# Performance work log

Hardware: AMD Instinct MI355X
Metric: run time of the kernel (lower is better)

Reference implementation:

```python
import jax, jax.numpy as jnp
import numpy as np

B, T, C, HR = 8, 4096, 256, 4
N_LAYER, LAYER_ID = 12, 3
HID = HR * C


def _fancy_decay_first():
    # Faithful reproduction of VRWKV_SpatialMix._init_weights(init_mode='fancy')
    r01 = LAYER_ID / (N_LAYER - 1)
    h = np.arange(C, dtype=np.float32)
    decay = -5.0 + 8.0 * (h / (C - 1)) ** (0.7 + 1.3 * r01)
    zig = ((np.arange(1, C + 1) % 3) - 1).astype(np.float32) * 0.5
    first = np.float32(np.log(0.3)) + zig
    return jnp.asarray(decay, jnp.float32), jnp.asarray(first, jnp.float32)


def setup_inputs() -> dict:
    key = jax.random.key(0)
    ks = jax.random.split(key, 12)
    s = 0.02  # small weight scale keeps exp(k) well-conditioned
    decay, first = _fancy_decay_first()
    return {
        "x": jax.random.normal(ks[0], (B, T, C), jnp.float32),
        "Wk": jax.random.normal(ks[1], (C, C), jnp.float32) * s,
        "Wv": jax.random.normal(ks[2], (C, C), jnp.float32) * s,
        "Wr": jax.random.normal(ks[3], (C, C), jnp.float32) * s,
        "Wo": jax.random.normal(ks[4], (C, C), jnp.float32) * s,
        "Wk_ffn": jax.random.normal(ks[5], (C, HID), jnp.float32) * s,
        "Wv_ffn": jax.random.normal(ks[6], (HID, C), jnp.float32) * s,
        "Wr_ffn": jax.random.normal(ks[7], (C, C), jnp.float32) * s,
        "g1": 1.0 + 0.1 * jax.random.normal(ks[8], (C,), jnp.float32),
        "b1": 0.1 * jax.random.normal(ks[9], (C,), jnp.float32),
        "g2": 1.0 + 0.1 * jax.random.normal(ks[10], (C,), jnp.float32),
        "b2": 0.1 * jax.random.normal(ks[11], (C,), jnp.float32),
        "spatial_decay": decay,
        "spatial_first": first,
    }


def _ln(x, g, b):
    m = jnp.mean(x, axis=-1, keepdims=True)
    v = jnp.var(x, axis=-1, keepdims=True)
    return (x - m) * jax.lax.rsqrt(v + 1e-5) * g + b


def _wkv(w, u, k, v):
    # Numerically-stable log-space WKV recurrence (same math as wkv_cuda):
    # y_t = (sum_{i<t} e^{w*(t-1-i)+k_i} v_i + e^{u+k_t} v_t)
    #     / (sum_{i<t} e^{w*(t-1-i)+k_i}     + e^{u+k_t})
    # w,u: [C]; k,v: [B,T,C] -> y: [B,T,C]
    Bb, Tt, Cc = k.shape
    kT = jnp.swapaxes(k, 0, 1)  # [T,B,C]
    vT = jnp.swapaxes(v, 0, 1)

    def step(carry, kv):
        p, q, o = carry           # [B,C] num / den / running max exponent
        kt, vt = kv               # [B,C]
        no = jnp.maximum(o, u + kt)
        A = jnp.exp(o - no)
        E = jnp.exp(u + kt - no)
        y = (A * p + E * vt) / (A * q + E)
        no2 = jnp.maximum(w + o, kt)
        A2 = jnp.exp(w + o - no2)
        E2 = jnp.exp(kt - no2)
        return (A2 * p + E2 * vt, A2 * q + E2, no2), y

    init = (jnp.zeros((Bb, Cc), k.dtype),
            jnp.zeros((Bb, Cc), k.dtype),
            jnp.full((Bb, Cc), -1e38, k.dtype))
    _, yT = jax.lax.scan(step, init, (kT, vT))
    return jnp.swapaxes(yT, 0, 1)


def reference(x, Wk, Wv, Wr, Wo, Wk_ffn, Wv_ffn, Wr_ffn, g1, b1, g2, b2,
              spatial_decay, spatial_first):
    Tlen = x.shape[1]
    # --- SpatialMix (shift_pixel=0 -> xk=xv=xr=h, key_norm=False) ---
    h = _ln(x, g1, b1)
    k = h @ Wk
    v = h @ Wv
    sr = jax.nn.sigmoid(h @ Wr)
    y = _wkv(spatial_decay / Tlen, spatial_first / Tlen, k, v)
    x = x + (sr * y) @ Wo
    # --- ChannelMix (square-ReLU MLP, sigmoid receptance gate) ---
    h2 = _ln(x, g2, b2)
    kk = jnp.square(jax.nn.relu(h2 @ Wk_ffn))
    x = x + jax.nn.sigmoid(h2 @ Wr_ffn) * (kk @ Wv_ffn)
    return x
```

## Files before the change

kernel.cpp:

```cpp
#include <hip/hip_runtime.h>
#include <hip/hip_bf16.h>
#include <math.h>

#define TDIM 4096
#define CDIM 256
#define BDIM 8
#define NTOK (BDIM * TDIM)
#define HIDDIM 1024
#define NCHUNK 256
#define CHLEN 16

typedef float f32x4 __attribute__((ext_vector_type(4)));
typedef __bf16 bf16x8 __attribute__((ext_vector_type(8)));
typedef __bf16 bf16x4 __attribute__((ext_vector_type(4)));
typedef long long i64x2 __attribute__((ext_vector_type(2)));

#define GLDS16(gp, lp) __builtin_amdgcn_global_load_lds( \
    (const __attribute__((address_space(1))) void*)(gp), \
    (__attribute__((address_space(3))) void*)(lp), 16, 0, 0)

#define WAITCNT_VM8  0x0F78
#define WAITCNT_VM5  0x0F75
#define WAITCNT_VM4  0x0F74
#define WAITCNT_VM2  0x0F72
#define WAITCNT_VM0  0x0F70
#define WAITCNT_LGKM0 0xC07F

#define STAGE_FENCE() do { \
    __builtin_amdgcn_sched_barrier(0); \
    __builtin_amdgcn_s_waitcnt(WAITCNT_LGKM0); \
    __builtin_amdgcn_s_barrier(); \
    __builtin_amdgcn_sched_barrier(0); \
  } while (0)

__device__ __forceinline__ float sigm(float v) { return 1.0f / (1.0f + __expf(-v)); }

__device__ __forceinline__ int permk(int k) {
  return (k & ~63) + (((k >> 3) & 3) << 4) + (((k >> 5) & 1) << 3) + (k & 7);
}

__global__ __launch_bounds__(256) void prep(
    const float* __restrict__ Wk, const float* __restrict__ Wv,
    const float* __restrict__ Wr, const float* __restrict__ Wo,
    const float* __restrict__ Wkf, const float* __restrict__ Wvf,
    const float* __restrict__ Wrf,
    __bf16* __restrict__ WoT, unsigned char* __restrict__ Wkvr8,
    unsigned char* __restrict__ Wkfr8, unsigned char* __restrict__ Wvf8,
    const float* __restrict__ x, const float* __restrict__ gamma,
    const float* __restrict__ beta, unsigned char* __restrict__ h8) {
  if (blockIdx.x >= 1024) {
    const int wave = threadIdx.x >> 6, lane = threadIdx.x & 63;
    const long long row = (long long)(blockIdx.x - 1024) * 4 + wave;
    const long long base = row * CDIM + lane * 4;
    const f32x4 v = *(const f32x4*)&x[base];
    float s = v[0] + v[1] + v[2] + v[3];
    float s2 = v[0]*v[0] + v[1]*v[1] + v[2]*v[2] + v[3]*v[3];
    #pragma unroll
    for (int o = 1; o < 64; o <<= 1) { s += __shfl_xor(s, o); s2 += __shfl_xor(s2, o); }
    const float mean = s * (1.0f / CDIM);
    const float var = s2 * (1.0f / CDIM) - mean * mean;
    const float rstd = rsqrtf(var + 1e-5f);
    const f32x4 g4 = *(const f32x4*)&gamma[lane * 4];
    const f32x4 b4 = *(const f32x4*)&beta[lane * 4];
    float o0 = (v[0] - mean) * rstd * g4[0] + b4[0];
    float o1 = (v[1] - mean) * rstd * g4[1] + b4[1];
    float o2 = (v[2] - mean) * rstd * g4[2] + b4[2];
    float o3 = (v[3] - mean) * rstd * g4[3] + b4[3];
    int w = 0;
    w = __builtin_amdgcn_cvt_pk_fp8_f32(o0, o1, w, false);
    w = __builtin_amdgcn_cvt_pk_fp8_f32(o2, o3, w, true);
    *(int*)&h8[row * CDIM + permk(lane * 4)] = w;
    return;
  }
  long long j = (long long)blockIdx.x * 256 + threadIdx.x;
  if (j < 49152) {
    const long long d = j * 4;
    const int n = (int)(d >> 8), k0 = (int)(d & 255);
    const float* src = (n < 256) ? Wk : (n < 512 ? Wv : Wr);
    const int nn = n & 255;
    int w = 0;
    w = __builtin_amdgcn_cvt_pk_fp8_f32(src[k0 * 256 + nn],
                                        src[(k0 + 1) * 256 + nn], w, false);
    w = __builtin_amdgcn_cvt_pk_fp8_f32(src[(k0 + 2) * 256 + nn],
                                        src[(k0 + 3) * 256 + nn], w, true);
    *(int*)&Wkvr8[(long long)n * 256 + permk(k0)] = w;
    return;
  }
  j -= 49152;
  if (j < 65536) { int n = (int)(j >> 8), k = (int)(j & 255);
    WoT[j] = (__bf16)Wo[k * 256 + n]; return; }
  j -= 65536;
  if (j < 81920) {
    const long long d = j * 4;
    const int n = (int)(d >> 8), k0 = (int)(d & 255);
    float v0, v1, v2, v3;
    if (n < 1024) {
      v0 = Wkf[(long long)k0 * 1024 + n];       v1 = Wkf[(long long)(k0 + 1) * 1024 + n];
      v2 = Wkf[(long long)(k0 + 2) * 1024 + n]; v3 = Wkf[(long long)(k0 + 3) * 1024 + n];
    } else {
      const int m = n - 1024;
      v0 = Wrf[k0 * 256 + m];       v1 = Wrf[(k0 + 1) * 256 + m];
      v2 = Wrf[(k0 + 2) * 256 + m]; v3 = Wrf[(k0 + 3) * 256 + m];
    }
    int w = 0;
    w = __builtin_amdgcn_cvt_pk_fp8_f32(v0, v1, w, false);
    w = __builtin_amdgcn_cvt_pk_fp8_f32(v2, v3, w, true);
    *(int*)&Wkfr8[(long long)n * 256 + permk(k0)] = w;
    return;
  }
  j -= 81920;
  if (j < 65536) {
    const long long d = j * 4;
    const int n = (int)(d >> 10), k0 = (int)(d & 1023);
    int w = 0;
    w = __builtin_amdgcn_cvt_pk_fp8_f32(Wvf[(long long)k0 * 256 + n],
                                        Wvf[(long long)(k0 + 1) * 256 + n], w, false);
    w = __builtin_amdgcn_cvt_pk_fp8_f32(Wvf[(long long)(k0 + 2) * 256 + n],
                                        Wvf[(long long)(k0 + 3) * 256 + n], w, true);
    *(int*)&Wvf8[(long long)n * 1024 + permk(k0)] = w;
    return;
  }
}

template <int EPI, int NY>
__global__ __launch_bounds__(512, 4) void gemmF(
    const unsigned char* __restrict__ A8, const unsigned char* __restrict__ B8,
    __bf16* __restrict__ outH, __bf16* __restrict__ outH2,
    unsigned char* __restrict__ outC) {
  constexpr int NTILES = 256 * NY;
  constexpr int TPB = NTILES / 512;
  static_assert(NTILES % 512 == 0, "grid divisibility");
  __shared__ unsigned char sA[2][4 * 8192];

  const int tid = threadIdx.x;
  const int wave = tid >> 6, lane = tid & 63;
  const int quad = lane >> 4, mrow = lane & 15;
  const int wm = (wave & 1) * 64, wn = (wave >> 1) * 32;
  const int srow = lane >> 2;
  const int o16 = (lane & 3) * 16;
  const int t0 = blockIdx.x * TPB;

  auto issueA = [&](int t, int buf) {
    const long long bm = (long long)(t & 255) * 128;
    const int r0 = wave * 16;
    #pragma unroll
    for (int g = 0; g < 4; g++)
      GLDS16(A8 + (bm + r0 + srow) * 256 + g * 64 + o16,
             &sA[buf][g * 8192 + r0 * 64]);
  };

  i64x2 fb[2][4];
  auto loadB = [&](int y) {
    const long long bn = (long long)y * 128;
    #pragma unroll
    for (int nt = 0; nt < 2; nt++)
      #pragma unroll
      for (int g = 0; g < 4; g++)
        fb[nt][g] = *(const i64x2*)
            &B8[(bn + wn + nt * 16 + mrow) * 256 + g * 64 + quad * 16];
  };

  issueA(t0, 0);
  int prevy = -1;

  #pragma unroll 1
  for (int i = 0; i < TPB; i++) {
    const int t = t0 + i;
    const int y = t >> 8;
    const bool ych = (y != prevy);
    prevy = y;

    if (i == 0)          __builtin_amdgcn_s_waitcnt(WAITCNT_VM0);
    else if (EPI == 0)   __builtin_amdgcn_s_waitcnt(WAITCNT_VM4);
    else                 __builtin_amdgcn_s_waitcnt(WAITCNT_VM2);
    __builtin_amdgcn_s_barrier();

    if (ych) loadB(y);
    if (i + 1 < TPB) issueA(t + 1, (i + 1) & 1);

    f32x4 acc[4][2] = {};
    const int buf = i & 1;
    #pragma unroll
    for (int g = 0; g < 4; g++) {
      i64x2 fa[4];
      #pragma unroll
      for (int mt = 0; mt < 4; mt++)
        fa[mt] = *(const i64x2*)
            &sA[buf][g * 8192 + (wm + mt * 16 + mrow) * 64 + quad * 16];
      #pragma unroll
      for (int c = 0; c < 2; c++)
        #pragma unroll
        for (int mt = 0; mt < 4; mt++)
          #pragma unroll
          for (int nt = 0; nt < 2; nt++)
            acc[mt][nt] = __builtin_amdgcn_mfma_f32_16x16x32_fp8_fp8(
                fb[nt][g][c], fa[mt][c], acc[mt][nt], 0, 0, 0);
    }

    __builtin_amdgcn_s_barrier();
    unsigned char* stg = &sA[buf][0];
    const long long bm = (long long)(t & 255) * 128;

    if (EPI == 0) {
      const int plane = y >> 1;
      #pragma unroll
      for (int mt = 0; mt < 4; mt++) {
        const int row = wm + mt * 16 + mrow;
        const int swz = (row & 7) << 4;
        #pragma unroll
        for (int nt = 0; nt < 2; nt++) {
          const f32x4 a = acc[mt][nt];
          bf16x4 v;
          if (plane == 2) {
            #pragma unroll
            for (int r = 0; r < 4; r++) v[r] = (__bf16)sigm(a[r]);
          } else {
            #pragma unroll
            for (int r = 0; r < 4; r++) v[r] = (__bf16)a[r];
          }
          const int cb2 = (wn + nt * 16 + quad * 4) * 2;
          *(bf16x4*)&stg[row * 256 + (cb2 ^ swz)] = v;
        }
      }
      STAGE_FENCE();
      char* ob = (char*)(outH + (long long)plane * (32768LL * 256));
      const int row = tid >> 2, qb = (tid & 3) * 64;
      const int swz = (row & 7) << 4;
      const long long gb = (bm + row) * 512 + (long long)(y & 1) * 256 + qb;
      #pragma unroll
      for (int c = 0; c < 4; c++) {
        const i64x2 d = *(const i64x2*)&stg[row * 256 + ((qb + c * 16) ^ swz)];
        *(i64x2*)&ob[gb + c * 16] = d;
      }
    } else {
      if (y < 8) {
        #pragma unroll
        for (int mt = 0; mt < 4; mt++) {
          const int row = wm + mt * 16 + mrow;
          const int swz = (row & 7) << 4;
          #pragma unroll
          for (int nt = 0; nt < 2; nt++) {
            const f32x4 a = acc[mt][nt];
            float q0 = a[0] > 0.0f ? a[0] : 0.0f;
            float q1 = a[1] > 0.0f ? a[1] : 0.0f;
            float q2 = a[2] > 0.0f ? a[2] : 0.0f;
            float q3 = a[3] > 0.0f ? a[3] : 0.0f;
            int w = 0;
            w = __builtin_amdgcn_cvt_pk_fp8_f32(q0 * q0, q1 * q1, w, false);
            w = __builtin_amdgcn_cvt_pk_fp8_f32(q2 * q2, q3 * q3, w, true);
            const int cbl = wn + nt * 16 + quad * 4;
            *(int*)&stg[row * 128 + (permk(cbl) ^ swz)] = w;
          }
        }
        STAGE_FENCE();
        const int row = tid >> 2, sb = (tid & 3) * 32;
        const int swz = (row & 7) << 4;
        const long long gb = (bm + row) * 1024 + (long long)y * 128 + sb;
        #pragma unroll
        for (int c = 0; c < 2; c++) {
          const i64x2 d = *(const i64x2*)&stg[row * 128 + ((sb + c * 16) ^ swz)];
          *(i64x2*)&outC[gb + c * 16] = d;
        }
      } else {
        #pragma unroll
        for (int mt = 0; mt < 4; mt++) {
          const int row = wm + mt * 16 + mrow;
          const int swz = (row & 7) << 4;
          #pragma unroll
          for (int nt = 0; nt < 2; nt++) {
            const f32x4 a = acc[mt][nt];
            bf16x4 v;
            #pragma unroll
            for (int r = 0; r < 4; r++) v[r] = (__bf16)sigm(a[r]);
            const int cb2 = (wn + nt * 16 + quad * 4) * 2;
            *(bf16x4*)&stg[row * 256 + (cb2 ^ swz)] = v;
          }
        }
        STAGE_FENCE();
        char* ob = (char*)outH2;
        const int row = tid >> 2, qb = (tid & 3) * 64;
        const int swz = (row & 7) << 4;
        const long long gb = (bm + row) * 512 + (long long)(y - 8) * 256 + qb;
        #pragma unroll
        for (int c = 0; c < 4; c++) {
          const i64x2 d = *(const i64x2*)&stg[row * 256 + ((qb + c * 16) ^ swz)];
          *(i64x2*)&ob[gb + c * 16] = d;
        }
      }
    }
  }
}

template <int K, int EPI>
__global__ __launch_bounds__(256, 3) void gemm9(
    const unsigned char* __restrict__ A8, const unsigned char* __restrict__ B8,
    int M, __bf16* __restrict__ outH, __bf16* __restrict__ outH2,
    unsigned char* __restrict__ outC,
    float* __restrict__ outF, const __bf16* __restrict__ srcH,
    const __bf16* __restrict__ gate) {
  constexpr int NIT = K / 64;
  __shared__ unsigned char sA[3][128 * 64];
  __shared__ unsigned char sB[3][128 * 64];
  const int tid = threadIdx.x;
  const int wave = tid >> 6, lane = tid & 63;
  const int quad = lane >> 4, mrow = lane & 15;
  const long long bm = (long long)blockIdx.x * 128;
  const long long bn = (long long)blockIdx.y * 128;
  const int wm = (wave & 1) * 64, wn = (wave >> 1) * 64;
  const int srow = lane >> 2;
  const int o16 = (lane & 3) * 16;

  auto issue = [&](int g) {
    const int buf = g % 3;
    const long long k0 = (long long)g * 64;
    const int a0 = wave * 32;
    GLDS16(A8 + (bm + a0 + srow) * (long long)K + k0 + o16, &sA[buf][a0 * 64]);
    GLDS16(A8 + (bm + a0 + 16 + srow) * (long long)K + k0 + o16, &sA[buf][(a0 + 16) * 64]);
    GLDS16(B8 + (bn + a0 + srow) * (long long)K + k0 + o16, &sB[buf][a0 * 64]);
    GLDS16(B8 + (bn + a0 + 16 + srow) * (long long)K + k0 + o16, &sB[buf][(a0 + 16) * 64]);
  };

  f32x4 acc[4][4] = {};
  issue(0);
  if (NIT > 1) issue(1);

  auto compute = [&](int g) {
    const int buf = g % 3;
    i64x2 fa[4], fb[4];
    #pragma unroll
    for (int mt = 0; mt < 4; mt++)
      fa[mt] = *(const i64x2*)&sA[buf][(wm + mt * 16 + mrow) * 64 + quad * 16];
    #pragma unroll
    for (int nt = 0; nt < 4; nt++)
      fb[nt] = *(const i64x2*)&sB[buf][(wn + nt * 16 + mrow) * 64 + quad * 16];
    #pragma unroll
    for (int c = 0; c < 2; c++)
      #pragma unroll
      for (int mt = 0; mt < 4; mt++)
        #pragma unroll
        for (int nt = 0; nt < 4; nt++)
          acc[mt][nt] = __builtin_amdgcn_mfma_f32_16x16x32_fp8_fp8(
              fb[nt][c], fa[mt][c], acc[mt][nt], 0, 0, 0);
  };

  #pragma unroll 1
  for (int g = 0; g < NIT; g++) {
    if (g == NIT - 1) {
      __builtin_amdgcn_s_waitcnt(WAITCNT_VM0);
    } else {
      __builtin_amdgcn_s_waitcnt(WAITCNT_VM4);
    }
    __builtin_amdgcn_s_barrier();
    if (g + 2 < NIT) issue(g + 2);
    compute(g);
  }

  #pragma unroll
  for (int mt = 0; mt < 4; mt++) {
    #pragma unroll
    for (int nt = 0; nt < 4; nt++) {
      const long long row = bm + wm + mt * 16 + mrow;
      const long long colb = bn + wn + nt * 16 + quad * 4;
      const f32x4 a = acc[mt][nt];
      const long long idx = row * 256 + colb;
      const bf16x4 s4 = *(const bf16x4*)&srcH[idx];
      const bf16x4 g4 = *(const bf16x4*)&gate[idx];
      f32x4 v;
      #pragma unroll
      for (int r = 0; r < 4; r++) v[r] = (float)s4[r] + (float)g4[r] * a[r];
      *(f32x4*)&outF[idx] = v;
    }
  }
}

__global__ __launch_bounds__(256, 2) void gemm7(
    const __bf16* __restrict__ A, const __bf16* __restrict__ Bt,
    const float* __restrict__ x,
    const float* __restrict__ gammaP, const float* __restrict__ betaP,
    __bf16* __restrict__ x1h, unsigned char* __restrict__ h28) {
  constexpr int K = 256;
  __shared__ __bf16 sA[3][64 * 32];
  __shared__ __bf16 sB[3][256 * 32];
  __shared__ float redS[4][64], redQ[4][64];

  const int tid = threadIdx.x;
  const int wave = tid >> 6, lane = tid & 63;
  const int quad = lane >> 4, mrow = lane & 15;
  const long long bm = (long long)blockIdx.x * 64;
  const int wn = wave * 64;
  const int lrow = lane >> 2;
  const int lk = (lane & 3) * 8;

  auto issue = [&](int g) {
    const int buf = g % 3;
    const long long k0 = (long long)g * 32;
    GLDS16(A + (bm + wave * 16 + lrow) * (long long)K + k0 + lk,
           &sA[buf][(wave * 16) * 32]);
    #pragma unroll
    for (int bc = 0; bc < 4; bc++) {
      const int r0 = wave * 64 + bc * 16;
      GLDS16(Bt + (r0 + lrow) * (long long)K + k0 + lk, &sB[buf][r0 * 32]);
    }
  };

  f32x4 acc[4][4] = {};

  auto compute = [&](int g) {
    const int buf = g % 3;
    bf16x8 fa[4], fb[4];
    #pragma unroll
    for (int mt = 0; mt < 4; mt++)
      fa[mt] = *(const bf16x8*)&sA[buf][(mt * 16 + mrow) * 32 + quad * 8];
    #pragma unroll
    for (int nt = 0; nt < 4; nt++)
      fb[nt] = *(const bf16x8*)&sB[buf][(wn + nt * 16 + mrow) * 32 + quad * 8];
    #pragma unroll
    for (int mt = 0; mt < 4; mt++)
      #pragma unroll
      for (int nt = 0; nt < 4; nt++)
        acc[mt][nt] = __builtin_amdgcn_mfma_f32_16x16x32_bf16(fb[nt], fa[mt], acc[mt][nt], 0, 0, 0);
  };

  issue(0);
  issue(1);
  #pragma unroll 1
  for (int g = 0; g < 8; g++) {
    if (g == 7) {
      __builtin_amdgcn_s_waitcnt(WAITCNT_VM0);
    } else {
      __builtin_amdgcn_s_waitcnt(WAITCNT_VM5);
    }
    __builtin_amdgcn_s_barrier();
    if (g + 2 < 8) issue(g + 2);
    compute(g);
  }

  float sum[4] = {0, 0, 0, 0}, sq[4] = {0, 0, 0, 0};
  #pragma unroll
  for (int mt = 0; mt < 4; mt++) {
    #pragma unroll
    for (int nt = 0; nt < 4; nt++) {
      const long long row = bm + mt * 16 + mrow;
      const long long colb = wn + nt * 16 + quad * 4;
      acc[mt][nt] += *(const f32x4*)&x[row * 256 + colb];
      #pragma unroll
      for (int r = 0; r < 4; r++) {
        sum[mt] += acc[mt][nt][r];
        sq[mt] += acc[mt][nt][r] * acc[mt][nt][r];
      }
    }
  }
  #pragma unroll
  for (int mt = 0; mt < 4; mt++) {
    sum[mt] += __shfl_xor(sum[mt], 16); sq[mt] += __shfl_xor(sq[mt], 16);
    sum[mt] += __shfl_xor(sum[mt], 32); sq[mt] += __shfl_xor(sq[mt], 32);
  }
  if (quad == 0) {
    #pragma unroll
    for (int mt = 0; mt < 4; mt++) {
      redS[wave][mt * 16 + mrow] = sum[mt];
      redQ[wave][mt * 16 + mrow] = sq[mt];
    }
  }
  __syncthreads();
  #pragma unroll
  for (int mt = 0; mt < 4; mt++) {
    const int rb = mt * 16 + mrow;
    const float ts = redS[0][rb] + redS[1][rb] + redS[2][rb] + redS[3][rb];
    const float tq = redQ[0][rb] + redQ[1][rb] + redQ[2][rb] + redQ[3][rb];
    const float mean = ts * (1.0f / 256.0f);
    const float rstd = rsqrtf(tq * (1.0f / 256.0f) - mean * mean + 1e-5f);
    const long long row = bm + rb;
    #pragma unroll
    for (int nt = 0; nt < 4; nt++) {
      const long long colb = wn + nt * 16 + quad * 4;
      const f32x4 g4 = *(const f32x4*)&gammaP[colb];
      const f32x4 b4 = *(const f32x4*)&betaP[colb];
      bf16x4 xo;
      const float t0 = acc[mt][nt][0], t1 = acc[mt][nt][1];
      const float t2 = acc[mt][nt][2], t3 = acc[mt][nt][3];
      xo[0] = (__bf16)t0; xo[1] = (__bf16)t1; xo[2] = (__bf16)t2; xo[3] = (__bf16)t3;
      const float h0 = (t0 - mean) * rstd * g4[0] + b4[0];
      const float h1 = (t1 - mean) * rstd * g4[1] + b4[1];
      const float h2v = (t2 - mean) * rstd * g4[2] + b4[2];
      const float h3 = (t3 - mean) * rstd * g4[3] + b4[3];
      *(bf16x4*)&x1h[row * 256 + colb] = xo;
      int w = 0;
      w = __builtin_amdgcn_cvt_pk_fp8_f32(h0, h1, w, false);
      w = __builtin_amdgcn_cvt_pk_fp8_f32(h2v, h3, w, true);
      *(int*)&h28[row * 256 + permk((int)colb)] = w;
    }
  }
}

__global__ __launch_bounds__(256) void wkv_phase1(
    const __bf16* __restrict__ ka, const __bf16* __restrict__ va,
    const float* __restrict__ decay,
    float* __restrict__ Sloc, float* __restrict__ Zloc) {
  const int wave = threadIdx.x >> 6, lane = threadIdx.x & 63;
  const int gi = blockIdx.x * 4 + wave;
  const int b = gi >> 8, chunk = gi & (NCHUNK - 1);
  const int c0 = lane * 4;
  const f32x4 w4 = *(const f32x4*)&decay[c0];
  f32x4 ew;
  #pragma unroll
  for (int r = 0; r < 4; r++) ew[r] = __expf(w4[r] * (1.0f / TDIM));
  f32x4 S = {0,0,0,0}, Z = {0,0,0,0};
  long long base = ((long long)b * TDIM + (long long)chunk * CHLEN) * 256 + c0;
  #pragma unroll 4
  for (int t = 0; t < CHLEN; t++) {
    const bf16x4 k4 = *(const bf16x4*)&ka[base + (long long)t * 256];
    const bf16x4 v4 = *(const bf16x4*)&va[base + (long long)t * 256];
    #pragma unroll
    for (int r = 0; r < 4; r++) {
      const float ek = __expf((float)k4[r]);
      S[r] = ew[r] * S[r] + ek * (float)v4[r];
      Z[r] = ew[r] * Z[r] + ek;
    }
  }
  const long long o = (long long)gi * 256 + c0;
  *(f32x4*)&Sloc[o] = S;
  *(f32x4*)&Zloc[o] = Z;
}

__global__ __launch_bounds__(256) void wkv_phase2(
    const float* __restrict__ Sloc, const float* __restrict__ Zloc,
    const float* __restrict__ decay,
    float* __restrict__ Sstart, float* __restrict__ Zstart) {
  const int idx = blockIdx.x * 256 + threadIdx.x;
  const int c = idx & 255;
  const int b = idx >> 8;
  const float w = decay[c] * (1.0f / TDIM);
  const float ewL = __expf(w * (float)CHLEN);
  float S = 0.0f, Z = 0.0f;
  for (int j = 0; j < NCHUNK; j++) {
    const long long o = ((long long)b * NCHUNK + j) * 256 + c;
    Sstart[o] = S;
    Zstart[o] = Z;
    S = ewL * S + Sloc[o];
    Z = ewL * Z + Zloc[o];
  }
}

__global__ __launch_bounds__(256) void wkv_phase3(
    const __bf16* __restrict__ ka, const __bf16* __restrict__ va,
    const __bf16* __restrict__ ra,
    const float* __restrict__ decay, const float* __restrict__ first,
    const float* __restrict__ Sstart, const float* __restrict__ Zstart,
    __bf16* __restrict__ a2) {
  const int wave = threadIdx.x >> 6, lane = threadIdx.x & 63;
  const int gi = blockIdx.x * 4 + wave;
  const int b = gi >> 8, chunk = gi & (NCHUNK - 1);
  const int c0 = lane * 4;
  const f32x4 w4 = *(const f32x4*)&decay[c0];
  const f32x4 u4 = *(const f32x4*)&first[c0];
  f32x4 ew, eu;
  #pragma unroll
  for (int r = 0; r < 4; r++) {
    ew[r] = __expf(w4[r] * (1.0f / TDIM));
    eu[r] = __expf(u4[r] * (1.0f / TDIM));
  }
  const long long so = (long long)gi * 256 + c0;
  f32x4 S = *(const f32x4*)&Sstart[so];
  f32x4 Z = *(const f32x4*)&Zstart[so];
  long long base = ((long long)b * TDIM + (long long)chunk * CHLEN) * 256 + c0;
  #pragma unroll 2
  for (int t = 0; t < CHLEN; t++) {
    const long long p = base + (long long)t * 256;
    const bf16x4 k4 = *(const bf16x4*)&ka[p];
    const bf16x4 v4 = *(const bf16x4*)&va[p];
    const bf16x4 r4 = *(const bf16x4*)&ra[p];
    bf16x4 o;
    #pragma unroll
    for (int r = 0; r < 4; r++) {
      const float ek = __expf((float)k4[r]);
      const float E = eu[r] * ek;
      const float y = (S[r] + E * (float)v4[r]) / (Z[r] + E);
      o[r] = (__bf16)((float)r4[r] * y);
      S[r] = ew[r] * S[r] + ek * (float)v4[r];
      Z[r] = ew[r] * Z[r] + ek;
    }
    *(bf16x4*)&a2[p] = o;
  }
}

extern "C" void kernel_launch(void* const* d_in, const int* in_sizes, int n_in,
                              void* d_out, int out_size, void* d_ws, size_t ws_size,
                              hipStream_t stream) {
  const float* x     = (const float*)d_in[0];
  const float* Wk    = (const float*)d_in[1];
  const float* Wv    = (const float*)d_in[2];
  const float* Wr    = (const float*)d_in[3];
  const float* Wo    = (const float*)d_in[4];
  const float* Wkf   = (const float*)d_in[5];
  const float* Wvf   = (const float*)d_in[6];
  const float* Wrf   = (const float*)d_in[7];
  const float* g1    = (const float*)d_in[8];
  const float* b1    = (const float*)d_in[9];
  const float* g2    = (const float*)d_in[10];
  const float* b2    = (const float*)d_in[11];
  const float* decay = (const float*)d_in[12];
  const float* first = (const float*)d_in[13];
  float* out = (float*)d_out;
  char* ws = (char*)d_ws;

  __bf16* ka     = (__bf16*)(ws + 0);
  __bf16* va     = (__bf16*)(ws + 16777216LL);
  __bf16* ra     = (__bf16*)(ws + 33554432LL);
  __bf16* a2     = (__bf16*)(ws + 50331648LL);
  __bf16* g2buf  = (__bf16*)(ws + 50331648LL);
  unsigned char* h8  = (unsigned char*)(ws + 67108864LL);
  unsigned char* h28 = (unsigned char*)(ws + 67108864LL);
  __bf16* x1h    = (__bf16*)(ws + 83886080LL);
  unsigned char* kk8 = (unsigned char*)(ws + 100663296LL);
  float*  Sloc   = (float*)(ws + 134217728LL);
  float*  Zloc   = (float*)(ws + 137363456LL);
  float*  Sstart = (float*)(ws + 140509184LL);
  float*  Zstart = (float*)(ws + 143654912LL);
  __bf16* WoT    = (__bf16*)(ws + 167772160LL);
  unsigned char* Wkvr8 = (unsigned char*)(ws + 167903232LL);
  unsigned char* Wkfr8 = (unsigned char*)(ws + 168099840LL);
  unsigned char* Wvf8  = (unsigned char*)(ws + 168427520LL);

  prep<<<1024 + NTOK / 4, 256, 0, stream>>>(
      Wk, Wv, Wr, Wo, Wkf, Wvf, Wrf, WoT, Wkvr8, Wkfr8, Wvf8,
      x, g1, b1, h8);

  gemmF<0, 6><<<512, 512, 0, stream>>>(h8, Wkvr8, ka, nullptr, nullptr);
  wkv_phase1<<<BDIM * NCHUNK / 4, 256, 0, stream>>>(ka, va, decay, Sloc, Zloc);
  wkv_phase2<<<BDIM, 256, 0, stream>>>(Sloc, Zloc, decay, Sstart, Zstart);
  wkv_phase3<<<BDIM * NCHUNK / 4, 256, 0, stream>>>(ka, va, ra, decay, first,
                                                    Sstart, Zstart, a2);
  gemm7<<<NTOK / 64, 256, 0, stream>>>(a2, WoT, x, g2, b2, x1h, h28);

  gemmF<2, 10><<<512, 512, 0, stream>>>(h28, Wkfr8, nullptr, g2buf, kk8);
  gemm9<1024, 3><<<dim3(NTOK / 128, 2), 256, 0, stream>>>(
      kk8, Wvf8, NTOK, nullptr, nullptr, nullptr, out, x1h, g2buf);
}
```

Before: 256.1 us.

## Split WKV chunk-prefix scan into segmented scan with carry fixup in phase3

The serial cross-chunk prefix scan, which ran on only 8 blocks over 256 chunks, is split into 8 segments per batch computed in parallel on 64 blocks. Each segment writes local prefixes and its total. Phase3 combines the preceding segment totals with the decay powers to rebuild the exact starting state. This shortens the latency-bound serial chain at the cost of a small extra loop and more exp calls in phase3.

```diff
diff --git a/kernel.cpp b/kernel.cpp
--- a/kernel.cpp
+++ b/kernel.cpp
@@ -9,6 +9,8 @@
 #define HIDDIM 1024
 #define NCHUNK 256
 #define CHLEN 16
+#define NSEG 8
+#define SEGCH 32
 
 typedef float f32x4 __attribute__((ext_vector_type(4)));
 typedef __bf16 bf16x8 __attribute__((ext_vector_type(8)));
@@ -523,34 +525,40 @@
   *(f32x4*)&Zloc[o] = Z;
 }
 
-__global__ __launch_bounds__(256) void wkv_phase2(
+__global__ __launch_bounds__(256) void wkv_phase2a(
     const float* __restrict__ Sloc, const float* __restrict__ Zloc,
     const float* __restrict__ decay,
-    float* __restrict__ Sstart, float* __restrict__ Zstart) {
-  const int idx = blockIdx.x * 256 + threadIdx.x;
-  const int c = idx & 255;
-  const int b = idx >> 8;
+    float* __restrict__ LprefS, float* __restrict__ LprefZ,
+    float* __restrict__ TS, float* __restrict__ TZ) {
+  const int b = blockIdx.x >> 3, seg = blockIdx.x & 7;
+  const int c = threadIdx.x;
   const float w = decay[c] * (1.0f / TDIM);
   const float ewL = __expf(w * (float)CHLEN);
   float S = 0.0f, Z = 0.0f;
-  for (int j = 0; j < NCHUNK; j++) {
-    const long long o = ((long long)b * NCHUNK + j) * 256 + c;
-    Sstart[o] = S;
-    Zstart[o] = Z;
+  long long o = ((long long)(b * NCHUNK + seg * SEGCH)) * 256 + c;
+  #pragma unroll 4
+  for (int i = 0; i < SEGCH; i++, o += 256) {
+    LprefS[o] = S;
+    LprefZ[o] = Z;
     S = ewL * S + Sloc[o];
     Z = ewL * Z + Zloc[o];
   }
+  const int to = (b * NSEG + seg) * 256 + c;
+  TS[to] = S;
+  TZ[to] = Z;
 }
 
 __global__ __launch_bounds__(256) void wkv_phase3(
     const __bf16* __restrict__ ka, const __bf16* __restrict__ va,
     const __bf16* __restrict__ ra,
     const float* __restrict__ decay, const float* __restrict__ first,
-    const float* __restrict__ Sstart, const float* __restrict__ Zstart,
+    const float* __restrict__ LprefS, const float* __restrict__ LprefZ,
+    const float* __restrict__ TS, const float* __restrict__ TZ,
     __bf16* __restrict__ a2) {
   const int wave = threadIdx.x >> 6, lane = threadIdx.x & 63;
   const int gi = blockIdx.x * 4 + wave;
   const int b = gi >> 8, chunk = gi & (NCHUNK - 1);
+  const int seg = chunk >> 5, d = chunk & (SEGCH - 1);
   const int c0 = lane * 4;
   const f32x4 w4 = *(const f32x4*)&decay[c0];
   const f32x4 u4 = *(const f32x4*)&first[c0];
@@ -561,8 +569,23 @@
     eu[r] = __expf(u4[r] * (1.0f / TDIM));
   }
   const long long so = (long long)gi * 256 + c0;
-  f32x4 S = *(const f32x4*)&Sstart[so];
-  f32x4 Z = *(const f32x4*)&Zstart[so];
+  const f32x4 Lp = *(const f32x4*)&LprefS[so];
+  const f32x4 LpZ = *(const f32x4*)&LprefZ[so];
+  f32x4 S, Z;
+  #pragma unroll
+  for (int r = 0; r < 4; r++) {
+    const float wr = w4[r] * (1.0f / TDIM);
+    const float ew32 = __expf(wr * (float)(CHLEN * SEGCH));
+    float CS = 0.0f, CZ = 0.0f;
+    const int tb = b * NSEG * 256 + c0 + r;
+    for (int s = 0; s < seg; s++) {
+      CS = ew32 * CS + TS[tb + s * 256];
+      CZ = ew32 * CZ + TZ[tb + s * 256];
+    }
+    const float f0 = __expf(wr * (float)(CHLEN * d));
+    S[r] = f0 * CS + Lp[r];
+    Z[r] = f0 * CZ + LpZ[r];
+  }
   long long base = ((long long)b * TDIM + (long long)chunk * CHLEN) * 256 + c0;
   #pragma unroll 2
   for (int t = 0; t < CHLEN; t++) {
@@ -615,8 +638,10 @@
   unsigned char* kk8 = (unsigned char*)(ws + 100663296LL);
   float*  Sloc   = (float*)(ws + 134217728LL);
   float*  Zloc   = (float*)(ws + 137363456LL);
-  float*  Sstart = (float*)(ws + 140509184LL);
-  float*  Zstart = (float*)(ws + 143654912LL);
+  float*  LprefS = (float*)(ws + 140509184LL);
+  float*  LprefZ = (float*)(ws + 143654912LL);
+  float*  TS     = (float*)(ws + 146800640LL);
+  float*  TZ     = (float*)(ws + 146866176LL);
   __bf16* WoT    = (__bf16*)(ws + 167772160LL);
   unsigned char* Wkvr8 = (unsigned char*)(ws + 167903232LL);
   unsigned char* Wkfr8 = (unsigned char*)(ws + 168099840LL);
@@ -628,9 +653,10 @@
 
   gemmF<0, 6><<<512, 512, 0, stream>>>(h8, Wkvr8, ka, nullptr, nullptr);
   wkv_phase1<<<BDIM * NCHUNK / 4, 256, 0, stream>>>(ka, va, decay, Sloc, Zloc);
-  wkv_phase2<<<BDIM, 256, 0, stream>>>(Sloc, Zloc, decay, Sstart, Zstart);
+  wkv_phase2a<<<BDIM * NSEG, 256, 0, stream>>>(Sloc, Zloc, decay,
+                                               LprefS, LprefZ, TS, TZ);
   wkv_phase3<<<BDIM * NCHUNK / 4, 256, 0, stream>>>(ka, va, ra, decay, first,
-                                                    Sstart, Zstart, a2);
+                                                    LprefS, LprefZ, TS, TZ, a2);
   gemm7<<<NTOK / 64, 256, 0, stream>>>(a2, WoT, x, g2, b2, x1h, h28);
 
   gemmF<2, 10><<<512, 512, 0, stream>>>(h28, Wkfr8, nullptr, g2buf, kk8);
```

After: 252.6 us. About the same (-1.4%).
